# Performance work log

Hardware: AMD Instinct MI355X
Metric: run time of the kernel (lower is better)

Reference implementation:

```python
import jax, jax.numpy as jnp
import numpy as np

N, NIN, NOUT = 8192, 512, 512


def setup_inputs() -> dict:
    key = jax.random.key(0)
    k1, k2, k3 = jax.random.split(key, 3)
    H = jax.random.normal(k1, (N, NIN), dtype=jnp.float32)
    adj_matrix = jax.random.uniform(k2, (N, N), dtype=jnp.float32)
    W = jax.random.normal(k3, (NOUT, NIN), dtype=jnp.float32) / np.sqrt(NIN)
    b = jnp.zeros((NOUT,), dtype=jnp.float32)
    return {"H": H, "adj_matrix": adj_matrix, "W": W, "b": b}


def reference(H, adj_matrix, W, b):
    n = adj_matrix.shape[0]
    # adj + I (self-loops)
    A = adj_matrix + jnp.eye(n, dtype=adj_matrix.dtype)
    # column degrees (torch.sum(dim=0))
    deg = jnp.sum(A, axis=0)
    d = deg ** -0.5
    d = jnp.where(jnp.isinf(d), 0.0, d)
    # D^-1/2 A D^-1/2 implemented as elementwise row/col rescale (same math as diag matmuls)
    A = d[:, None] * A * d[None, :]
    # message passing + linear (torch Linear: x @ W.T + b) + tanh
    Hm = A @ H  # [N, nin]
    out = jnp.tanh(Hm @ W.T + b)
    return out
```

## Files before the change

### kernel.cpp

```cpp
#include <hip/hip_runtime.h>
#include <hip/hip_bf16.h>

#define N_NODES 8192
#define N_IN 512
#define N_OUT 512

typedef __bf16 bf16;
typedef __bf16 bf16x4 __attribute__((ext_vector_type(4)));
typedef __bf16 bf16x8 __attribute__((ext_vector_type(8)));
typedef float f32x4 __attribute__((ext_vector_type(4)));

__device__ __forceinline__ void gload16(const void* g, void* l) {
  __builtin_amdgcn_global_load_lds((const __attribute__((address_space(1))) void*)g,
                                   (__attribute__((address_space(3))) void*)l, 16, 0, 0);
}

#define WAITVM(N) asm volatile("s_waitcnt vmcnt(" #N ")" ::: "memory")
#define BAR() do { asm volatile("" ::: "memory"); __builtin_amdgcn_s_barrier(); \
                   asm volatile("" ::: "memory"); } while (0)
#define SCHED0() __builtin_amdgcn_sched_barrier(0)
#define LGKM0() asm volatile("s_waitcnt lgkmcnt(0)" ::: "memory")

__global__ __launch_bounds__(256) void k_colsum_cvt(const float* __restrict__ adj,
                                                    bf16* __restrict__ adjb,
                                                    float* __restrict__ partial) {
  const int tid  = threadIdx.x;
  const int col0 = blockIdx.x * 1024 + tid * 4;
  const int row0 = blockIdx.y * 64;
  float s0 = 0.f, s1 = 0.f, s2 = 0.f, s3 = 0.f;
#pragma unroll 4
  for (int r = 0; r < 64; ++r) {
    float4 v = *reinterpret_cast<const float4*>(adj + (size_t)(row0 + r) * N_NODES + col0);
    s0 += v.x; s1 += v.y; s2 += v.z; s3 += v.w;
    const int dq = row0 + r - col0;
    if ((unsigned)dq < 4u) reinterpret_cast<float*>(&v)[dq] += 1.0f;
    bf16x4 o = { (bf16)v.x, (bf16)v.y, (bf16)v.z, (bf16)v.w };
    *reinterpret_cast<bf16x4*>(adjb + (size_t)(row0 + r) * N_NODES + col0) = o;
  }
  float4 ps = { s0, s1, s2, s3 };
  *reinterpret_cast<float4*>(partial + (size_t)blockIdx.y * N_NODES + col0) = ps;
}

__global__ __launch_bounds__(256) void k_dvec(const float* __restrict__ partial,
                                              float* __restrict__ dv) {
  const int j = blockIdx.x * 256 + threadIdx.x;
  float s = 1.0f;
#pragma unroll 8
  for (int p = 0; p < 128; ++p) s += partial[(size_t)p * N_NODES + j];
  dv[j] = rsqrtf(s);
}

__global__ __launch_bounds__(256) void k_hst(const float* __restrict__ H,
                                             const float* __restrict__ dv,
                                             bf16* __restrict__ Hst) {
  __shared__ float t[64][65];
  const int tid = threadIdx.x;
  const int j0 = blockIdx.x * 64;
  const int k0 = blockIdx.y * 64;
  const int rr = tid >> 4;
  const int cc = (tid & 15) * 4;
#pragma unroll
  for (int p = 0; p < 4; ++p) {
    const int r = p * 16 + rr;
    const float d = dv[j0 + r];
    float4 v = *reinterpret_cast<const float4*>(H + (size_t)(j0 + r) * N_IN + k0 + cc);
    t[r][cc + 0] = v.x * d; t[r][cc + 1] = v.y * d;
    t[r][cc + 2] = v.z * d; t[r][cc + 3] = v.w * d;
  }
  __syncthreads();
#pragma unroll
  for (int p = 0; p < 4; ++p) {
    const int kr = p * 16 + rr;
    bf16x4 o = { (bf16)t[cc + 0][kr], (bf16)t[cc + 1][kr],
                 (bf16)t[cc + 2][kr], (bf16)t[cc + 3][kr] };
    *reinterpret_cast<bf16x4*>(Hst + (size_t)(k0 + kr) * N_NODES + j0 + cc) = o;
  }
}

__global__ __launch_bounds__(256) void k_wcvt(const float* __restrict__ W, bf16* __restrict__ Wb) {
  const int i = (blockIdx.x * 256 + threadIdx.x) * 4;
  float4 v = *reinterpret_cast<const float4*>(W + i);
  bf16x4 o = { (bf16)v.x, (bf16)v.y, (bf16)v.z, (bf16)v.w };
  *reinterpret_cast<bf16x4*>(Wb + i) = o;
}

template<int KDIM, int NSPLIT>
__global__ __launch_bounds__(512, 2) void k_gemm256(
    const bf16* __restrict__ A, const bf16* __restrict__ B, bf16* __restrict__ P) {
  constexpr int KSEG = KDIM / NSPLIT;
  constexpr int NT = KSEG / 64;
  constexpr int NIT = NT / 2;
  constexpr int NBLK = 64 * NSPLIT;
  __shared__ __attribute__((aligned(128))) char lds[2 * 65536];

  const int bid = blockIdx.x;
  const int l = (bid & 7) * (NBLK / 8) + (bid >> 3);
  const int split = l / 64;
  const int rem = l % 64;
  const int bm0 = (rem >> 1) * 256;
  const int bn0 = (rem & 1) * 256;

  const int tid = threadIdx.x;
  const int lane = tid & 63;
  const int wid = tid >> 6;
  const int wr = wid >> 2;
  const int wc = wid & 3;

  const int srow = tid >> 3;
  const int sslot = (tid & 7) ^ (srow & 7);
  const size_t koff = (size_t)split * KSEG;
  const int wuni = wid * 1024;

  auto GA = [&](int k, int h, int buf) {
    const bf16* g = A + (size_t)(bm0 + h * 128 + srow) * KDIM + koff + (size_t)k * 64 + sslot * 8;
    char* d = lds + buf * 65536 + h * 16384 + wuni;
    gload16(g, d);
    gload16(g + (size_t)64 * KDIM, d + 8192);
  };
  auto GB = [&](int k, int h, int buf) {
    const bf16* g = B + (size_t)(bn0 + h * 128 + srow) * KDIM + koff + (size_t)k * 64 + sslot * 8;
    char* d = lds + buf * 65536 + 32768 + h * 16384 + wuni;
    gload16(g, d);
    gload16(g + (size_t)64 * KDIM, d + 8192);
  };

  const int frow = lane & 15;
  const int fk = lane >> 4;
  const int e7 = lane & 7;
  const int sb0 = ((fk) ^ e7) << 4;
  const int sb1 = ((4 + fk) ^ e7) << 4;
  const int aBase = wr * 16384 + frow * 128;
  const int bBase = 32768 + (wc >> 1) * 16384 + ((wc & 1) * 64 + frow) * 128;

  f32x4 acc[8][4] = {};
  bf16x8 av[2][4], bv0[2][2], bv1[2][2];

#define LDA(BUF, MH)                                                          \
  do {                                                                        \
    const char* lb_ = lds + (BUF) * 65536;                                    \
    _Pragma("unroll") for (int m = 0; m < 4; ++m) {                           \
      av[0][m] = *(const bf16x8*)(lb_ + aBase + ((MH) * 4 + m) * 2048 + sb0); \
      av[1][m] = *(const bf16x8*)(lb_ + aBase + ((MH) * 4 + m) * 2048 + sb1); \
    }                                                                         \
  } while (0)
#define LDB(BUF, NH, BV)                                                      \
  do {                                                                        \
    const char* lb_ = lds + (BUF) * 65536;                                    \
    _Pragma("unroll") for (int n = 0; n < 2; ++n) {                           \
      BV[0][n] = *(const bf16x8*)(lb_ + bBase + ((NH) * 2 + n) * 2048 + sb0); \
      BV[1][n] = *(const bf16x8*)(lb_ + bBase + ((NH) * 2 + n) * 2048 + sb1); \
    }                                                                         \
  } while (0)
#define MFMA16(MH, NH, BV)                                                    \
  do {                                                                        \
    _Pragma("unroll") for (int kk = 0; kk < 2; ++kk)                          \
    _Pragma("unroll") for (int m = 0; m < 4; ++m)                             \
    _Pragma("unroll") for (int n = 0; n < 2; ++n)                             \
      acc[(MH) * 4 + m][(NH) * 2 + n] = __builtin_amdgcn_mfma_f32_16x16x32_bf16( \
          av[kk][m], BV[kk][n], acc[(MH) * 4 + m][(NH) * 2 + n], 0, 0, 0);    \
  } while (0)

#define PH_OPEN()  do { SCHED0(); __builtin_amdgcn_s_barrier(); LGKM0(); SCHED0(); \
                        __builtin_amdgcn_s_setprio(1); } while (0)
#define PH_CLOSE() do { __builtin_amdgcn_s_setprio(0); SCHED0(); \
                        __builtin_amdgcn_s_barrier(); SCHED0(); } while (0)
#define PH_CLOSE_F(WV) do { __builtin_amdgcn_s_setprio(0); SCHED0(); WV; \
                            __builtin_amdgcn_s_barrier(); SCHED0(); } while (0)

  GB(0, 0, 0); GB(0, 1, 0); GA(0, 0, 0); GA(0, 1, 0);
  GB(1, 0, 1); GB(1, 1, 1);
  WAITVM(4);
  BAR();

#pragma unroll 1
  for (int i = 0; i < NIT; ++i) {
    const int t = 2 * i;
    const bool s2 = (t + 2 < NT);
    const bool s3 = (t + 3 < NT);
    LDA(0, 0); LDB(0, 0, bv0);
    GA(t + 1, 0, 1);
    PH_OPEN(); MFMA16(0, 0, bv0); PH_CLOSE();
    LDB(0, 1, bv1);
    GA(t + 1, 1, 1);
    PH_OPEN(); MFMA16(0, 1, bv1); PH_CLOSE();
    LDA(0, 1);
    if (s2) GB(t + 2, 0, 0);
    PH_OPEN(); MFMA16(1, 1, bv1); PH_CLOSE();
    if (s2) GB(t + 2, 1, 0);
    PH_OPEN(); MFMA16(1, 0, bv0);
    if (s2) { PH_CLOSE_F(WAITVM(4)); } else { PH_CLOSE_F(WAITVM(0)); }
    LDA(1, 0); LDB(1, 0, bv0);
    if (s2) GA(t + 2, 0, 0);
    PH_OPEN(); MFMA16(0, 0, bv0); PH_CLOSE();
    LDB(1, 1, bv1);
    if (s2) GA(t + 2, 1, 0);
    PH_OPEN(); MFMA16(0, 1, bv1); PH_CLOSE();
    LDA(1, 1);
    if (s3) GB(t + 3, 0, 1);
    PH_OPEN(); MFMA16(1, 1, bv1); PH_CLOSE();
    if (s3) GB(t + 3, 1, 1);
    PH_OPEN(); MFMA16(1, 0, bv0);
    if (s3) { PH_CLOSE_F(WAITVM(4)); } else { PH_CLOSE_F(WAITVM(0)); }
  }
#undef LDA
#undef LDB
#undef MFMA16
#undef PH_OPEN
#undef PH_CLOSE
#undef PH_CLOSE_F

#pragma unroll
  for (int m = 0; m < 8; ++m) {
#pragma unroll
    for (int j = 0; j < 4; ++j) {
      const int grow = bm0 + wr * 128 + m * 16 + (lane >> 4) * 4 + j;
      bf16* prow = P + (size_t)split * ((size_t)N_NODES * N_IN) + (size_t)grow * N_IN;
#pragma unroll
      for (int n = 0; n < 4; ++n) {
        const int gcol = bn0 + wc * 64 + n * 16 + (lane & 15);
        prow[gcol] = (bf16)acc[m][n][j];
      }
    }
  }
}

template<int KDIM>
__global__ __launch_bounds__(256, 2) void k_gemm(
    const bf16* __restrict__ A, const bf16* __restrict__ B,
    const float* __restrict__ bias, float* __restrict__ outf) {
  constexpr int NT = KDIM / 64;
  constexpr int NBLK = 256;
  __shared__ __attribute__((aligned(128))) char lds[2 * 32768];

  const int bid = blockIdx.x;
  const int logical = (bid & 7) * (NBLK / 8) + (bid >> 3);
  const int bm0 = (logical >> 2) * 128;
  const int bn0 = (logical & 3) * 128;

  const int tid = threadIdx.x;
  const int wid = tid >> 6;
  const int lane = tid & 63;
  const int wr = wid & 1, wc = wid >> 1;

  const int srow = tid >> 3;
  const int scol = ((tid & 7) ^ (srow & 7)) << 3;
  const size_t a_src = (size_t)(bm0 + srow) * KDIM + scol;
  const size_t b_src = (size_t)(bn0 + srow) * KDIM + scol;

  const int frow = lane & 15;
  const int fk = lane >> 4;
  const int swz = (lane & 7) << 4;
  const int a_row_byte = (wr * 64 + frow) * 128;
  const int b_row_byte = 16384 + (wc * 64 + frow) * 128;

  f32x4 acc[4][4] = {};

  auto stage = [&](int t) {
    char* lbase = lds + (t & 1) * 32768;
    const bf16* ag = A + a_src + (size_t)t * 64;
    const bf16* bg = B + b_src + (size_t)t * 64;
#pragma unroll
    for (int ch = 0; ch < 4; ++ch) {
      gload16(ag + (size_t)(ch * 32) * KDIM, lbase + ch * 4096 + wid * 1024);
      gload16(bg + (size_t)(ch * 32) * KDIM, lbase + 16384 + ch * 4096 + wid * 1024);
    }
  };

  auto compute = [&](int t) {
    const char* lbase = lds + (t & 1) * 32768;
#pragma unroll
    for (int kk = 0; kk < 2; ++kk) {
      const int colb = (kk * 64 + fk * 16) ^ swz;
      bf16x8 av[4], bv[4];
#pragma unroll
      for (int m = 0; m < 4; ++m)
        av[m] = *reinterpret_cast<const bf16x8*>(lbase + a_row_byte + m * 2048 + colb);
#pragma unroll
      for (int n = 0; n < 4; ++n)
        bv[n] = *reinterpret_cast<const bf16x8*>(lbase + b_row_byte + n * 2048 + colb);
#pragma unroll
      for (int m = 0; m < 4; ++m)
#pragma unroll
        for (int n = 0; n < 4; ++n)
          acc[m][n] = __builtin_amdgcn_mfma_f32_16x16x32_bf16(av[m], bv[n], acc[m][n], 0, 0, 0);
    }
  };

  stage(0);
#pragma unroll 1
  for (int t = 0; t < NT - 1; ++t) {
    stage(t + 1);
    WAITVM(8);
    BAR();
    compute(t);
    BAR();
  }
  WAITVM(0);
  BAR();
  compute(NT - 1);

#pragma unroll
  for (int m = 0; m < 4; ++m) {
#pragma unroll
    for (int j = 0; j < 4; ++j) {
      const int grow = bm0 + wr * 64 + m * 16 + (lane >> 4) * 4 + j;
      float* orow = outf + (size_t)grow * N_OUT;
#pragma unroll
      for (int n = 0; n < 4; ++n) {
        const int gcol = bn0 + wc * 64 + n * 16 + (lane & 15);
        float v = acc[m][n][j] + bias[gcol];
        v = fminf(fmaxf(v, -15.f), 15.f);
        const float e = __expf(2.f * v);
        orow[gcol] = (e - 1.f) / (e + 1.f);
      }
    }
  }
}

__global__ __launch_bounds__(256) void k_red(const bf16* __restrict__ P,
                                             const float* __restrict__ dv,
                                             bf16* __restrict__ Hm) {
  const int t = blockIdx.x * 256 + threadIdx.x;
  const int row = t >> 6;
  const int col = (t & 63) << 3;
  const size_t off = (size_t)row * N_IN + col;
  constexpr size_t S = (size_t)N_NODES * N_IN;
  const float d = dv[row];
  const bf16x8 p0 = *reinterpret_cast<const bf16x8*>(P + off);
  const bf16x8 p1 = *reinterpret_cast<const bf16x8*>(P + S + off);
  const bf16x8 p2 = *reinterpret_cast<const bf16x8*>(P + 2 * S + off);
  const bf16x8 p3 = *reinterpret_cast<const bf16x8*>(P + 3 * S + off);
  bf16x8 o;
#pragma unroll
  for (int e = 0; e < 8; ++e)
    o[e] = (bf16)(d * (((float)p0[e] + (float)p1[e]) + ((float)p2[e] + (float)p3[e])));
  *reinterpret_cast<bf16x8*>(Hm + off) = o;
}

extern "C" void kernel_launch(void* const* d_in, const int* in_sizes, int n_in,
                              void* d_out, int out_size, void* d_ws, size_t ws_size,
                              hipStream_t stream) {
  const float* H   = (const float*)d_in[0];
  const float* adj = (const float*)d_in[1];
  const float* W   = (const float*)d_in[2];
  const float* b   = (const float*)d_in[3];
  float* out = (float*)d_out;
  char* ws = (char*)d_ws;

  bf16*  adjb = (bf16*)(ws);
  bf16*  Hst  = (bf16*)(ws + 134217728);
  bf16*  Hm   = (bf16*)(ws + 142606336);
  bf16*  Wb   = (bf16*)(ws + 150994944);
  float* part = (float*)(ws + 151519232);
  float* dv   = (float*)(ws + 155713536);
  bf16*  P    = (bf16*)(ws + 155746304);

  k_colsum_cvt<<<dim3(8, 128), 256, 0, stream>>>(adj, adjb, part);
  k_dvec<<<32, 256, 0, stream>>>(part, dv);
  k_hst<<<dim3(128, 8), 256, 0, stream>>>(H, dv, Hst);
  k_wcvt<<<256, 256, 0, stream>>>(W, Wb);
  k_gemm256<8192, 4><<<256, 512, 0, stream>>>(adjb, Hst, P);
  k_red<<<2048, 256, 0, stream>>>(P, dv, Hm);
  k_gemm<512><<<256, 256, 0, stream>>>(Hm, Wb, b, out);
}
```

Before: 196.7 us.

## Fuse split-K reduction into second GEMM and merge W conversion with dvec

The split-K partial sums are now reduced, scaled by the degree vector, and written straight into LDS as the A operand of the second GEMM. This removes the separate reduction kernel and the global round trip through Hm. The W bf16 conversion is also folded into the degree-vector kernel, saving another launch. In exchange, each second-GEMM block re-reads P through registers instead of asynchronous LDS loads, because each N-column block reads the same rows. The pipeline also switches to plain __syncthreads with less load/compute overlap.

```diff
diff --git a/kernel.cpp b/kernel.cpp
--- a/kernel.cpp
+++ b/kernel.cpp
@@ -41,13 +41,24 @@
   *reinterpret_cast<float4*>(partial + (size_t)blockIdx.y * N_NODES + col0) = ps;
 }
 
-__global__ __launch_bounds__(256) void k_dvec(const float* __restrict__ partial,
-                                              float* __restrict__ dv) {
-  const int j = blockIdx.x * 256 + threadIdx.x;
-  float s = 1.0f;
+__global__ __launch_bounds__(256) void k_dvec_wcvt(const float* __restrict__ partial,
+                                                   float* __restrict__ dv,
+                                                   const float* __restrict__ W,
+                                                   bf16* __restrict__ Wb) {
+  const int b = blockIdx.x;
+  const int tid = threadIdx.x;
+  if (b < 32) {
+    const int j = b * 256 + tid;
+    float s = 1.0f;
 #pragma unroll 8
-  for (int p = 0; p < 128; ++p) s += partial[(size_t)p * N_NODES + j];
-  dv[j] = rsqrtf(s);
+    for (int p = 0; p < 128; ++p) s += partial[(size_t)p * N_NODES + j];
+    dv[j] = rsqrtf(s);
+  } else {
+    const int i = ((b - 32) * 256 + tid) * 4;
+    float4 v = *reinterpret_cast<const float4*>(W + i);
+    bf16x4 o = { (bf16)v.x, (bf16)v.y, (bf16)v.z, (bf16)v.w };
+    *reinterpret_cast<bf16x4*>(Wb + i) = o;
+  }
 }
 
 __global__ __launch_bounds__(256) void k_hst(const float* __restrict__ H,
@@ -75,13 +86,6 @@
                  (bf16)t[cc + 2][kr], (bf16)t[cc + 3][kr] };
     *reinterpret_cast<bf16x4*>(Hst + (size_t)(k0 + kr) * N_NODES + j0 + cc) = o;
   }
-}
-
-__global__ __launch_bounds__(256) void k_wcvt(const float* __restrict__ W, bf16* __restrict__ Wb) {
-  const int i = (blockIdx.x * 256 + threadIdx.x) * 4;
-  float4 v = *reinterpret_cast<const float4*>(W + i);
-  bf16x4 o = { (bf16)v.x, (bf16)v.y, (bf16)v.z, (bf16)v.w };
-  *reinterpret_cast<bf16x4*>(Wb + i) = o;
 }
 
 template<int KDIM, int NSPLIT>
@@ -224,12 +228,14 @@
   }
 }
 
-template<int KDIM>
-__global__ __launch_bounds__(256, 2) void k_gemm(
-    const bf16* __restrict__ A, const bf16* __restrict__ B,
-    const float* __restrict__ bias, float* __restrict__ outf) {
+__global__ __launch_bounds__(256, 2) void k_gemm2red(
+    const bf16* __restrict__ P, const bf16* __restrict__ Wb,
+    const float* __restrict__ dv, const float* __restrict__ bias,
+    float* __restrict__ outf) {
+  constexpr int KDIM = N_IN;
   constexpr int NT = KDIM / 64;
   constexpr int NBLK = 256;
+  constexpr size_t S = (size_t)N_NODES * N_IN;
   __shared__ __attribute__((aligned(128))) char lds[2 * 32768];
 
   const int bid = blockIdx.x;
@@ -242,10 +248,14 @@
   const int lane = tid & 63;
   const int wr = wid & 1, wc = wid >> 1;
 
+  const int arow = tid >> 1;
+  const int ar7 = arow & 7;
+  const float dscale = dv[bm0 + arow];
+  const bf16* pG = P + (size_t)(bm0 + arow) * N_IN + (tid & 1) * 32;
+
   const int srow = tid >> 3;
-  const int scol = ((tid & 7) ^ (srow & 7)) << 3;
-  const size_t a_src = (size_t)(bm0 + srow) * KDIM + scol;
-  const size_t b_src = (size_t)(bn0 + srow) * KDIM + scol;
+  const int sslot = (tid & 7) ^ (srow & 7);
+  const bf16* bG = Wb + (size_t)(bn0 + srow) * KDIM + sslot * 8;
 
   const int frow = lane & 15;
   const int fk = lane >> 4;
@@ -255,17 +265,30 @@
 
   f32x4 acc[4][4] = {};
 
-  auto stage = [&](int t) {
-    char* lbase = lds + (t & 1) * 32768;
-    const bf16* ag = A + a_src + (size_t)t * 64;
-    const bf16* bg = B + b_src + (size_t)t * 64;
-#pragma unroll
-    for (int ch = 0; ch < 4; ++ch) {
-      gload16(ag + (size_t)(ch * 32) * KDIM, lbase + ch * 4096 + wid * 1024);
-      gload16(bg + (size_t)(ch * 32) * KDIM, lbase + 16384 + ch * 4096 + wid * 1024);
+  auto stageB = [&](int t) {
+    char* lb = lds + (t & 1) * 32768 + 16384;
+    const bf16* g = bG + (size_t)t * 64;
+#pragma unroll
+    for (int c = 0; c < 4; ++c)
+      gload16(g + (size_t)(c * 32) * KDIM, lb + c * 4096 + wid * 1024);
+  };
+  auto stageA = [&](int t) {
+    char* lb = lds + (t & 1) * 32768;
+    const bf16* g = pG + (size_t)t * 64;
+#pragma unroll
+    for (int q = 0; q < 4; ++q) {
+      const bf16x8 p0 = *reinterpret_cast<const bf16x8*>(g + q * 8);
+      const bf16x8 p1 = *reinterpret_cast<const bf16x8*>(g + S + q * 8);
+      const bf16x8 p2 = *reinterpret_cast<const bf16x8*>(g + 2 * S + q * 8);
+      const bf16x8 p3 = *reinterpret_cast<const bf16x8*>(g + 3 * S + q * 8);
+      bf16x8 o;
+#pragma unroll
+      for (int e = 0; e < 8; ++e)
+        o[e] = (bf16)(dscale * (((float)p0[e] + (float)p1[e]) + ((float)p2[e] + (float)p3[e])));
+      const int slot = ((tid & 1) * 4 + q) ^ ar7;
+      *reinterpret_cast<bf16x8*>(lb + arow * 128 + slot * 16) = o;
     }
   };
-
   auto compute = [&](int t) {
     const char* lbase = lds + (t & 1) * 32768;
 #pragma unroll
@@ -286,18 +309,14 @@
     }
   };
 
-  stage(0);
+  stageB(0); stageA(0);
+  __syncthreads();
 #pragma unroll 1
-  for (int t = 0; t < NT - 1; ++t) {
-    stage(t + 1);
-    WAITVM(8);
-    BAR();
+  for (int t = 0; t < NT; ++t) {
+    if (t + 1 < NT) { stageB(t + 1); stageA(t + 1); }
     compute(t);
-    BAR();
-  }
-  WAITVM(0);
-  BAR();
-  compute(NT - 1);
+    __syncthreads();
+  }
 
 #pragma unroll
   for (int m = 0; m < 4; ++m) {
@@ -315,26 +334,6 @@
       }
     }
   }
-}
-
-__global__ __launch_bounds__(256) void k_red(const bf16* __restrict__ P,
-                                             const float* __restrict__ dv,
-                                             bf16* __restrict__ Hm) {
-  const int t = blockIdx.x * 256 + threadIdx.x;
-  const int row = t >> 6;
-  const int col = (t & 63) << 3;
-  const size_t off = (size_t)row * N_IN + col;
-  constexpr size_t S = (size_t)N_NODES * N_IN;
-  const float d = dv[row];
-  const bf16x8 p0 = *reinterpret_cast<const bf16x8*>(P + off);
-  const bf16x8 p1 = *reinterpret_cast<const bf16x8*>(P + S + off);
-  const bf16x8 p2 = *reinterpret_cast<const bf16x8*>(P + 2 * S + off);
-  const bf16x8 p3 = *reinterpret_cast<const bf16x8*>(P + 3 * S + off);
-  bf16x8 o;
-#pragma unroll
-  for (int e = 0; e < 8; ++e)
-    o[e] = (bf16)(d * (((float)p0[e] + (float)p1[e]) + ((float)p2[e] + (float)p3[e])));
-  *reinterpret_cast<bf16x8*>(Hm + off) = o;
 }
 
 extern "C" void kernel_launch(void* const* d_in, const int* in_sizes, int n_in,
@@ -349,17 +348,14 @@
 
   bf16*  adjb = (bf16*)(ws);
   bf16*  Hst  = (bf16*)(ws + 134217728);
-  bf16*  Hm   = (bf16*)(ws + 142606336);
-  bf16*  Wb   = (bf16*)(ws + 150994944);
-  float* part = (float*)(ws + 151519232);
-  float* dv   = (float*)(ws + 155713536);
-  bf16*  P    = (bf16*)(ws + 155746304);
+  bf16*  Wb   = (bf16*)(ws + 142606336);
+  float* part = (float*)(ws + 143130624);
+  float* dv   = (float*)(ws + 147324928);
+  bf16*  P    = (bf16*)(ws + 147357696);
 
   k_colsum_cvt<<<dim3(8, 128), 256, 0, stream>>>(adj, adjb, part);
-  k_dvec<<<32, 256, 0, stream>>>(part, dv);
+  k_dvec_wcvt<<<288, 256, 0, stream>>>(part, dv, W, Wb);
   k_hst<<<dim3(128, 8), 256, 0, stream>>>(H, dv, Hst);
-  k_wcvt<<<256, 256, 0, stream>>>(W, Wb);
   k_gemm256<8192, 4><<<256, 512, 0, stream>>>(adjb, Hst, P);
-  k_red<<<2048, 256, 0, stream>>>(P, dv, Hm);
-  k_gemm<512><<<256, 256, 0, stream>>>(Hm, Wb, b, out);
-}
+  k_gemm2red<<<256, 256, 0, stream>>>(P, Wb, dv, b, out);
+}
```

Result: slower. 206.1 us (+4.8%).
